# Optimization experiments

Measured on AMD Instinct MI355X. Metric: run time of the kernel, lower is better.

Reference implementation:

```python
import jax, jax.numpy as jnp
import numpy as np

B, A, C, G = 32, 5, 20, 19
TPER = 8  # targets per image -> T = B*TPER = 256
ANCHORS = np.array([[1.3221, 1.73145], [3.19275, 4.00944], [5.05587, 8.09892],
                    [9.47112, 4.84053], [11.2364, 10.0071]], dtype=np.float32)
OBJECT_SCALE, NOOBJECT_SCALE, CLASS_SCALE, COORD_SCALE = 5.0, 1.0, 1.0, 1.0
THRESH = 0.6


def _wh_iou_np(anc, wh):
    inter = np.minimum(anc[:, 0:1], wh[None, :, 0]) * np.minimum(anc[:, 1:2], wh[None, :, 1])
    union = anc[:, 0:1] * anc[:, 1:2] + wh[None, :, 0] * wh[None, :, 1] - inter
    return inter / (union + 1e-16)


def setup_inputs() -> dict:
    rng = np.random.default_rng(0)
    rows = []
    for b in range(B):
        cells = rng.choice(G * G, TPER, replace=False)  # distinct grid cells per image
        for c in cells:
            gy, gx = divmod(int(c), G)
            u, v = rng.uniform(0.05, 0.95, 2)
            w, h = rng.uniform(1.0, 8.0, 2) / G  # 1..8 grid units, in 0..1 image coords
            rows.append([b, rng.integers(C), (gx + u) / G, (gy + v) / G, w, h])
    t = np.array(rows, dtype=np.float32)
    # sort targets into (sample, anchor, gy, gx) mask order so mask-order gathers
    # line up with target-row order (as the original torch code implicitly assumes)
    wh_g = t[:, 4:6] * G
    ai = np.argmax(_wh_iou_np(ANCHORS, wh_g), axis=0)
    gx = (t[:, 2] * G).astype(np.int64)
    gy = (t[:, 3] * G).astype(np.int64)
    flat = ((t[:, 0].astype(np.int64) * A + ai) * G + gy) * G + gx
    t = t[np.argsort(flat)]
    x = jax.random.normal(jax.random.key(0), (B, A * (C + 5), G, G), dtype=jnp.float32) * 0.5
    return {"x": x, "targets": jnp.asarray(t), "seen": 0}


def _bbox_iou(b1, b2):
    # center-format boxes, last dim = (x, y, w, h); broadcasts over leading dims
    b1x1 = b1[..., 0] - b1[..., 2] / 2; b1x2 = b1[..., 0] + b1[..., 2] / 2
    b1y1 = b1[..., 1] - b1[..., 3] / 2; b1y2 = b1[..., 1] + b1[..., 3] / 2
    b2x1 = b2[..., 0] - b2[..., 2] / 2; b2x2 = b2[..., 0] + b2[..., 2] / 2
    b2y1 = b2[..., 1] - b2[..., 3] / 2; b2y2 = b2[..., 1] + b2[..., 3] / 2
    iw = jnp.clip(jnp.minimum(b1x2, b2x2) - jnp.maximum(b1x1, b2x1), 0.0)
    ih = jnp.clip(jnp.minimum(b1y2, b2y2) - jnp.maximum(b1y1, b2y1), 0.0)
    inter = iw * ih
    union = b1[..., 2] * b1[..., 3] + b2[..., 2] * b2[..., 3] - inter
    return inter / (union + 1e-16)


def _forward(x, targets, seen):
    anchors = jnp.asarray(ANCHORS)
    xp = x.reshape(B, A, C + 5, G, G).transpose(0, 1, 3, 4, 2)  # (B,A,G,G,C+5)
    tx, ty, tw, th = xp[..., 0], xp[..., 1], xp[..., 2], xp[..., 3]
    pred_conf = jax.nn.sigmoid(xp[..., 4])
    pred_cls = jax.nn.sigmoid(xp[..., 5:])
    tgs = targets[:, 2:6] * G  # (T,4) in grid units
    # anchor assignment via wh-iou (argmax over anchors)
    inter = jnp.minimum(anchors[:, 0:1], tgs[None, :, 2]) * jnp.minimum(anchors[:, 1:2], tgs[None, :, 3])
    wh_iou = inter / (anchors[:, 0:1] * anchors[:, 1:2] + tgs[None, :, 2] * tgs[None, :, 3] - inter)
    ai = jnp.argmax(wh_iou, axis=0)
    gx = tgs[:, 0].astype(jnp.int32); gy = tgs[:, 1].astype(jnp.int32)
    si = targets[:, 0].astype(jnp.int32); ci = targets[:, 1].astype(jnp.int32)
    # decode full grid
    gridx = jnp.arange(G, dtype=x.dtype)[None, None, None, :]
    gridy = jnp.arange(G, dtype=x.dtype)[None, None, :, None]
    sx, sy = jax.nn.sigmoid(tx), jax.nn.sigmoid(ty)
    pw = jnp.exp(tw) * anchors[:, 0][None, :, None, None]
    ph = jnp.exp(th) * anchors[:, 1][None, :, None, None]
    pred_boxes = jnp.stack([sx + gridx, sy + gridy, pw, ph], axis=-1)  # (B,A,G,G,4)
    T = targets.shape[0]
    target_mask = jnp.zeros((B, A, G, G), bool).at[si, ai, gy, gx].set(True)
    # losses at the T target locations (targets pre-sorted into mask order)
    iou_t = _bbox_iou(pred_boxes[si, ai, gy, gx], tgs)  # (T,)
    loss_cls = jnp.mean((pred_cls[si, ai, gy, gx] - jax.nn.one_hot(ci, C, dtype=x.dtype)) ** 2) * CLASS_SCALE
    tconf = iou_t  # rescore == 1: target_conf = 1 * iou
    loss_obj = jnp.mean((pred_conf[si, ai, gy, gx] - tconf) ** 2) * OBJECT_SCALE
    tcoords = jnp.stack([tgs[:, 0] - gx, tgs[:, 1] - gy,
                         jnp.log(tgs[:, 2] / anchors[ai, 0]),
                         jnp.log(tgs[:, 3] / anchors[ai, 1])], axis=-1)  # (T,4)
    pcoords_t = jnp.stack([sx[si, ai, gy, gx], sy[si, ai, gy, gx],
                           tw[si, ai, gy, gx], th[si, ai, gy, gx]], axis=-1)
    scale = jnp.sqrt(2.0 - tgs[:, 2] * tgs[:, 3] / (G * G))[:, None]
    loss_coords = jnp.mean(((pcoords_t - tcoords) * scale) ** 2) * COORD_SCALE
    # noobject mask: any-target IoU > thresh suppresses the noobj penalty (chunked over targets)
    CHUNK = 32
    tchunks = tgs.reshape(T // CHUNK, CHUNK, 4)
    def body(mx, tc):
        iou = _bbox_iou(pred_boxes[None], tc[:, None, None, None, None, :])  # (CHUNK,B,A,G,G)
        return jnp.maximum(mx, iou.max(0)), None
    max_iou, _ = jax.lax.scan(body, jnp.zeros((B, A, G, G), x.dtype), tchunks)
    noobj = (~target_mask) & (max_iou <= THRESH)
    ncnt = jnp.sum(noobj)
    loss_noobj = jnp.sum(jnp.where(noobj, pred_conf ** 2, 0.0)) / ncnt * NOOBJECT_SCALE
    total = loss_cls + loss_obj + loss_coords + loss_noobj
    if seen < 12800:
        prior = jnp.array([0.5, 0.5, 0.0, 0.0], x.dtype)
        pcoords = jnp.stack([sx, sy, tw, th], axis=-1)  # (B,A,G,G,4)
        nm = ~target_mask
        loss_prior = jnp.sum(jnp.where(nm[..., None], (pcoords - prior) ** 2, 0.0)) / (jnp.sum(nm) * 4) * 0.01
        total = total + loss_prior
    return total


def reference(x, targets, seen):
    return _forward(x, targets, seen)
```

## Files before the change

kernel.cpp:

```cpp
#include <hip/hip_runtime.h>
#include <math.h>

#define NB 32
#define NA 5
#define NC 20
#define NG 19
#define NT 256
#define GG  (NG*NG)
#define CELLS (NB*NA*NG*NG)
#define CPB 64
#define NBLK ((CELLS + CPB - 1)/CPB)
#define NWAVE 4
#define NTHR 256

#define OBJECT_SCALE   5.0f
#define NOOBJ_SCALE    1.0f
#define CLASS_SCALE    1.0f
#define COORD_SCALE    1.0f

__constant__ float c_aw[5] = {1.3221f, 3.19275f, 5.05587f, 9.47112f, 11.2364f};
__constant__ float c_ah[5] = {1.73145f, 4.00944f, 8.09892f, 4.84053f, 10.0071f};

__device__ __forceinline__ float sigm(float v) { return 1.f / (1.f + expf(-v)); }

#define SUMS_OFF 0
#define PART_OFF 16

__global__ __launch_bounds__(NTHR)
void k_main(const float* __restrict__ x, const float* __restrict__ tg,
            float* __restrict__ ws_f, float* __restrict__ partials) {
    __shared__ float4 s_corn[NT];
    __shared__ float  s_s06[NT];
    __shared__ int    s_mask[CPB];
    __shared__ float  s_pm[NWAVE][CPB];
    __shared__ float  s_wred[12];

    const int t = threadIdx.x;
    const int wave = t >> 6, lane = t & 63;
    const int cellBase = blockIdx.x * CPB;
    const int idx = cellBase + lane;
    const bool valid = idx < CELLS;

    float txv = 0.f, tyv = 0.f, twv = 0.f, thv = 0.f, cfv = 0.f;
    int ca = 0, cgx = 0, cgy = 0;
    if (valid) {
        int gx = idx % NG;
        int r  = idx / NG;
        int gy = r % NG;  r /= NG;
        int a  = r % NA;
        int b  = r / NA;
        ca = a; cgx = gx; cgy = gy;
        int base = ((b*NA + a)*(NC+5))*GG + gy*NG + gx;
        txv = x[base + 0*GG];
        tyv = x[base + 1*GG];
        twv = x[base + 2*GG];
        thv = x[base + 3*GG];
        cfv = x[base + 4*GG];
    }
    if (t < CPB) s_mask[t] = 0;

    const float2* tg2 = (const float2*)tg;
    float2 p0 = tg2[t*3+0], p1 = tg2[t*3+1], p2 = tg2[t*3+2];
    const float gxf = p1.x * NG, gyf = p1.y * NG;
    const float gw  = p2.x * NG, gh  = p2.y * NG;
    const int si = (int)p0.x, ci = (int)p0.y;
    int ai = 0;
    {
        float best = -1.f;
        #pragma unroll
        for (int a = 0; a < NA; ++a) {
            float inter = fminf(c_aw[a], gw) * fminf(c_ah[a], gh);
            float uni   = c_aw[a]*c_ah[a] + gw*gh - inter;
            float iou   = inter / uni;
            if (iou > best) { best = iou; ai = a; }
        }
    }
    const int gxi = (int)gxf, gyi = (int)gyf;
    const int fid = ((si*NA + ai)*NG + gyi)*NG + gxi;
    {
        float hw = gw*0.5f, hh = gh*0.5f;
        s_corn[t] = make_float4(gxf - hw, gyf - hh, gxf + hw, gyf + hh);
        s_s06[t]  = 0.6f * (gw * gh);
    }
    __syncthreads();

    {
        int rel = fid - cellBase;
        if (rel >= 0 && rel < CPB) s_mask[rel] = 1;
    }
    float bx1 = 1e30f, by1 = 1e30f, bx2 = 1e30f, by2 = 1e30f, cthr = 0.f;
    float sx = 0.f, sy = 0.f;
    if (valid) {
        sx = sigm(txv); sy = sigm(tyv);
        float pw = expf(twv) * c_aw[ca], ph = expf(thv) * c_ah[ca];
        float cx = sx + (float)cgx, cy = sy + (float)cgy;
        bx1 = cx - pw*0.5f; bx2 = cx + pw*0.5f;
        by1 = cy - ph*0.5f; by2 = cy + ph*0.5f;
        cthr = 0.6f * (pw * ph) + 6e-17f;
    }
    __syncthreads();

    float m0 = -1e30f, m1 = -1e30f;
    #pragma unroll 8
    for (int i = 0; i < 32; ++i) {
        int j0 = (i << 3) + wave;
        int j1 = j0 + 4;
        float4 ta = s_corn[j0];
        float sa = s_s06[j0];
        float4 tb = s_corn[j1];
        float sb = s_s06[j1];
        float iwa = fmaxf(fminf(bx2, ta.z) - fmaxf(bx1, ta.x), 0.f);
        float iha = fmaxf(fminf(by2, ta.w) - fmaxf(by1, ta.y), 0.f);
        float iwb = fmaxf(fminf(bx2, tb.z) - fmaxf(bx1, tb.x), 0.f);
        float ihb = fmaxf(fminf(by2, tb.w) - fmaxf(by1, tb.y), 0.f);
        m0 = fmaxf(m0, fmaf(1.6f, iwa * iha, -sa));
        m1 = fmaxf(m1, fmaf(1.6f, iwb * ihb, -sb));
    }
    s_pm[wave][lane] = fmaxf(m0, m1);
    __syncthreads();

    if (wave == 0) {
        float mm = fmaxf(fmaxf(s_pm[0][lane], s_pm[1][lane]),
                         fmaxf(s_pm[2][lane], s_pm[3][lane]));
        float v_no = 0.f, v_nc = 0.f, v_pr = 0.f, v_nm = 0.f;
        if (valid && !s_mask[lane]) {
            v_nm = 1.f;
            float e0 = sx - 0.5f, e1 = sy - 0.5f;
            v_pr = e0*e0 + e1*e1 + twv*twv + thv*thv;
            if (!(mm > cthr)) {
                float pc = sigm(cfv);
                v_no = pc * pc;
                v_nc = 1.f;
            }
        }
        #pragma unroll
        for (int off = 32; off > 0; off >>= 1) {
            v_no += __shfl_down(v_no, off);
            v_nc += __shfl_down(v_nc, off);
            v_pr += __shfl_down(v_pr, off);
            v_nm += __shfl_down(v_nm, off);
        }
        if (lane == 0) {
            partials[blockIdx.x*4 + 0] = v_no;
            partials[blockIdx.x*4 + 1] = v_nc;
            partials[blockIdx.x*4 + 2] = v_pr;
            partials[blockIdx.x*4 + 3] = v_nm;
        }
    }

    if (blockIdx.x == 0) {
        int base = ((si*NA + ai)*(NC+5))*GG + gyi*NG + gxi;
        float txt = x[base + 0*GG];
        float tyt = x[base + 1*GG];
        float twt = x[base + 2*GG];
        float tht = x[base + 3*GG];
        float cft = x[base + 4*GG];
        float tsx = sigm(txt), tsy = sigm(tyt);
        float aw = c_aw[ai], ah = c_ah[ai];
        float pw = expf(twt) * aw, ph = expf(tht) * ah;

        float pcx = tsx + (float)gxi, pcy = tsy + (float)gyi;
        float hw = gw*0.5f, hh = gh*0.5f;
        float iw = fmaxf(0.f, fminf(pcx + pw*0.5f, gxf + hw) - fmaxf(pcx - pw*0.5f, gxf - hw));
        float ih = fmaxf(0.f, fminf(pcy + ph*0.5f, gyf + hh) - fmaxf(pcy - ph*0.5f, gyf - hh));
        float inter = iw * ih;
        float uni = pw*ph + gw*gh - inter;
        float iou = inter / (uni + 1e-16f);

        float pconf = sigm(cft);
        float dobj = pconf - iou;
        float s_obj = dobj * dobj;

        float s_cls = 0.f;
        for (int cc = 0; cc < NC; ++cc) {
            float pc = sigm(x[base + (5 + cc)*GG]);
            float d = pc - ((cc == ci) ? 1.f : 0.f);
            s_cls += d * d;
        }

        float scl = sqrtf(2.f - gw*gh / (float)(NG*NG));
        float d0 = (tsx - (gxf - (float)gxi)) * scl;
        float d1 = (tsy - (gyf - (float)gyi)) * scl;
        float d2 = (twt - logf(gw / aw)) * scl;
        float d3 = (tht - logf(gh / ah)) * scl;
        float s_crd = d0*d0 + d1*d1 + d2*d2 + d3*d3;

        #pragma unroll
        for (int off = 32; off > 0; off >>= 1) {
            s_cls += __shfl_down(s_cls, off);
            s_obj += __shfl_down(s_obj, off);
            s_crd += __shfl_down(s_crd, off);
        }
        if (lane == 0) {
            s_wred[wave*3 + 0] = s_cls;
            s_wred[wave*3 + 1] = s_obj;
            s_wred[wave*3 + 2] = s_crd;
        }
        __syncthreads();
        if (t == 0) {
            ws_f[SUMS_OFF + 0] = s_wred[0] + s_wred[3] + s_wred[6] + s_wred[9];
            ws_f[SUMS_OFF + 1] = s_wred[1] + s_wred[4] + s_wred[7] + s_wred[10];
            ws_f[SUMS_OFF + 2] = s_wred[2] + s_wred[5] + s_wred[8] + s_wred[11];
        }
    }
}

__global__ __launch_bounds__(256)
void k_final(const float* __restrict__ ws_f, const float* __restrict__ partials,
             const int* __restrict__ seen, float* __restrict__ out) {
    int t = threadIdx.x;
    float a0 = 0.f, a1 = 0.f, a2 = 0.f, a3 = 0.f;
    for (int j = t; j < NBLK; j += 256) {
        a0 += partials[j*4 + 0];
        a1 += partials[j*4 + 1];
        a2 += partials[j*4 + 2];
        a3 += partials[j*4 + 3];
    }
    __shared__ float r0[256], r1[256], r2[256], r3[256];
    r0[t] = a0; r1[t] = a1; r2[t] = a2; r3[t] = a3;
    __syncthreads();
    for (int s = 128; s > 0; s >>= 1) {
        if (t < s) { r0[t]+=r0[t+s]; r1[t]+=r1[t+s]; r2[t]+=r2[t+s]; r3[t]+=r3[t+s]; }
        __syncthreads();
    }
    if (t == 0) {
        float loss_cls = ws_f[SUMS_OFF + 0] / (float)(NT * NC) * CLASS_SCALE;
        float loss_obj = ws_f[SUMS_OFF + 1] / (float)NT * OBJECT_SCALE;
        float loss_crd = ws_f[SUMS_OFF + 2] / (float)(NT * 4) * COORD_SCALE;
        float loss_no  = r0[0] / r1[0] * NOOBJ_SCALE;
        float total = loss_cls + loss_obj + loss_crd + loss_no;
        if (seen[0] < 12800) {
            total += r2[0] / (r3[0] * 4.f) * 0.01f;
        }
        out[0] = total;
    }
}

extern "C" void kernel_launch(void* const* d_in, const int* in_sizes, int n_in,
                              void* d_out, int out_size, void* d_ws, size_t ws_size,
                              hipStream_t stream) {
    const float* x    = (const float*)d_in[0];
    const float* tg   = (const float*)d_in[1];
    const int*   seen = (const int*)d_in[2];
    float* out  = (float*)d_out;
    float* ws_f = (float*)d_ws;
    float* partials = ws_f + PART_OFF;

    k_main<<<NBLK, NTHR, 0, stream>>>(x, tg, ws_f, partials);
    k_final<<<1, 256, 0, stream>>>(ws_f, partials, seen, out);
}
```

Measured before the change: 18.45 us.

## Double waves per block for IoU scan and use shuffle reduction in final kernel

Raises the main kernel from 4 to 8 waves per 64-cell block, so each wave scans half as many targets in the max-IoU loop. Only the first 256 threads load targets and compute target losses. The anchor argmax now compares by cross-multiplication instead of dividing. The final kernel reads partials as float4 and reduces with wave shuffles instead of a shared-memory tree. The trade-off is larger blocks with more idle threads in the target phases, which may lower occupancy.

```diff
diff --git a/kernel.cpp b/kernel.cpp
--- a/kernel.cpp
+++ b/kernel.cpp
@@ -10,8 +10,8 @@
 #define CELLS (NB*NA*NG*NG)
 #define CPB 64
 #define NBLK ((CELLS + CPB - 1)/CPB)
-#define NWAVE 4
-#define NTHR 256
+#define NWAVE 8
+#define NTHR (NWAVE*64)
 
 #define OBJECT_SCALE   5.0f
 #define NOOBJ_SCALE    1.0f
@@ -59,32 +59,32 @@
     }
     if (t < CPB) s_mask[t] = 0;
 
-    const float2* tg2 = (const float2*)tg;
-    float2 p0 = tg2[t*3+0], p1 = tg2[t*3+1], p2 = tg2[t*3+2];
-    const float gxf = p1.x * NG, gyf = p1.y * NG;
-    const float gw  = p2.x * NG, gh  = p2.y * NG;
-    const int si = (int)p0.x, ci = (int)p0.y;
-    int ai = 0;
-    {
-        float best = -1.f;
+    float gxf = 0.f, gyf = 0.f, gw = 0.f, gh = 0.f;
+    int si = 0, ci = 0, ai = 0, gxi = 0, gyi = 0, fid = -1;
+    if (t < NT) {
+        const float2* tg2 = (const float2*)tg;
+        float2 p0 = tg2[t*3+0], p1 = tg2[t*3+1], p2 = tg2[t*3+2];
+        gxf = p1.x * NG; gyf = p1.y * NG;
+        gw  = p2.x * NG; gh  = p2.y * NG;
+        si = (int)p0.x; ci = (int)p0.y;
+        float tarea = gw * gh;
+        float b_inter = fminf(c_aw[0], gw) * fminf(c_ah[0], gh);
+        float b_uni   = c_aw[0]*c_ah[0] + tarea - b_inter;
         #pragma unroll
-        for (int a = 0; a < NA; ++a) {
+        for (int a = 1; a < NA; ++a) {
             float inter = fminf(c_aw[a], gw) * fminf(c_ah[a], gh);
-            float uni   = c_aw[a]*c_ah[a] + gw*gh - inter;
-            float iou   = inter / uni;
-            if (iou > best) { best = iou; ai = a; }
-        }
-    }
-    const int gxi = (int)gxf, gyi = (int)gyf;
-    const int fid = ((si*NA + ai)*NG + gyi)*NG + gxi;
-    {
+            float uni   = c_aw[a]*c_ah[a] + tarea - inter;
+            if (inter * b_uni > b_inter * uni) { b_inter = inter; b_uni = uni; ai = a; }
+        }
+        gxi = (int)gxf; gyi = (int)gyf;
+        fid = ((si*NA + ai)*NG + gyi)*NG + gxi;
         float hw = gw*0.5f, hh = gh*0.5f;
         s_corn[t] = make_float4(gxf - hw, gyf - hh, gxf + hw, gyf + hh);
-        s_s06[t]  = 0.6f * (gw * gh);
-    }
-    __syncthreads();
-
-    {
+        s_s06[t]  = 0.6f * tarea;
+    }
+    __syncthreads();
+
+    if (t < NT) {
         int rel = fid - cellBase;
         if (rel >= 0 && rel < CPB) s_mask[rel] = 1;
     }
@@ -101,10 +101,10 @@
     __syncthreads();
 
     float m0 = -1e30f, m1 = -1e30f;
-    #pragma unroll 8
-    for (int i = 0; i < 32; ++i) {
-        int j0 = (i << 3) + wave;
-        int j1 = j0 + 4;
+    #pragma unroll
+    for (int i = 0; i < 16; ++i) {
+        int j0 = (i << 4) + wave;
+        int j1 = j0 + 8;
         float4 ta = s_corn[j0];
         float sa = s_s06[j0];
         float4 tb = s_corn[j1];
@@ -120,8 +120,9 @@
     __syncthreads();
 
     if (wave == 0) {
-        float mm = fmaxf(fmaxf(s_pm[0][lane], s_pm[1][lane]),
-                         fmaxf(s_pm[2][lane], s_pm[3][lane]));
+        float mm = s_pm[0][lane];
+        #pragma unroll
+        for (int w = 1; w < NWAVE; ++w) mm = fmaxf(mm, s_pm[w][lane]);
         float v_no = 0.f, v_nc = 0.f, v_pr = 0.f, v_nm = 0.f;
         if (valid && !s_mask[lane]) {
             v_nm = 1.f;
@@ -149,52 +150,54 @@
     }
 
     if (blockIdx.x == 0) {
-        int base = ((si*NA + ai)*(NC+5))*GG + gyi*NG + gxi;
-        float txt = x[base + 0*GG];
-        float tyt = x[base + 1*GG];
-        float twt = x[base + 2*GG];
-        float tht = x[base + 3*GG];
-        float cft = x[base + 4*GG];
-        float tsx = sigm(txt), tsy = sigm(tyt);
-        float aw = c_aw[ai], ah = c_ah[ai];
-        float pw = expf(twt) * aw, ph = expf(tht) * ah;
-
-        float pcx = tsx + (float)gxi, pcy = tsy + (float)gyi;
-        float hw = gw*0.5f, hh = gh*0.5f;
-        float iw = fmaxf(0.f, fminf(pcx + pw*0.5f, gxf + hw) - fmaxf(pcx - pw*0.5f, gxf - hw));
-        float ih = fmaxf(0.f, fminf(pcy + ph*0.5f, gyf + hh) - fmaxf(pcy - ph*0.5f, gyf - hh));
-        float inter = iw * ih;
-        float uni = pw*ph + gw*gh - inter;
-        float iou = inter / (uni + 1e-16f);
-
-        float pconf = sigm(cft);
-        float dobj = pconf - iou;
-        float s_obj = dobj * dobj;
-
-        float s_cls = 0.f;
-        for (int cc = 0; cc < NC; ++cc) {
-            float pc = sigm(x[base + (5 + cc)*GG]);
-            float d = pc - ((cc == ci) ? 1.f : 0.f);
-            s_cls += d * d;
-        }
-
-        float scl = sqrtf(2.f - gw*gh / (float)(NG*NG));
-        float d0 = (tsx - (gxf - (float)gxi)) * scl;
-        float d1 = (tsy - (gyf - (float)gyi)) * scl;
-        float d2 = (twt - logf(gw / aw)) * scl;
-        float d3 = (tht - logf(gh / ah)) * scl;
-        float s_crd = d0*d0 + d1*d1 + d2*d2 + d3*d3;
-
-        #pragma unroll
-        for (int off = 32; off > 0; off >>= 1) {
-            s_cls += __shfl_down(s_cls, off);
-            s_obj += __shfl_down(s_obj, off);
-            s_crd += __shfl_down(s_crd, off);
-        }
-        if (lane == 0) {
-            s_wred[wave*3 + 0] = s_cls;
-            s_wred[wave*3 + 1] = s_obj;
-            s_wred[wave*3 + 2] = s_crd;
+        float s_cls = 0.f, s_obj = 0.f, s_crd = 0.f;
+        if (t < NT) {
+            int base = ((si*NA + ai)*(NC+5))*GG + gyi*NG + gxi;
+            float txt = x[base + 0*GG];
+            float tyt = x[base + 1*GG];
+            float twt = x[base + 2*GG];
+            float tht = x[base + 3*GG];
+            float cft = x[base + 4*GG];
+            float tsx = sigm(txt), tsy = sigm(tyt);
+            float aw = c_aw[ai], ah = c_ah[ai];
+            float pw = expf(twt) * aw, ph = expf(tht) * ah;
+
+            float pcx = tsx + (float)gxi, pcy = tsy + (float)gyi;
+            float hw = gw*0.5f, hh = gh*0.5f;
+            float iw = fmaxf(0.f, fminf(pcx + pw*0.5f, gxf + hw) - fmaxf(pcx - pw*0.5f, gxf - hw));
+            float ih = fmaxf(0.f, fminf(pcy + ph*0.5f, gyf + hh) - fmaxf(pcy - ph*0.5f, gyf - hh));
+            float inter = iw * ih;
+            float uni = pw*ph + gw*gh - inter;
+            float iou = inter / (uni + 1e-16f);
+
+            float pconf = sigm(cft);
+            float dobj = pconf - iou;
+            s_obj = dobj * dobj;
+
+            for (int cc = 0; cc < NC; ++cc) {
+                float pc = sigm(x[base + (5 + cc)*GG]);
+                float d = pc - ((cc == ci) ? 1.f : 0.f);
+                s_cls += d * d;
+            }
+
+            float scl = sqrtf(2.f - gw*gh / (float)(NG*NG));
+            float d0 = (tsx - (gxf - (float)gxi)) * scl;
+            float d1 = (tsy - (gyf - (float)gyi)) * scl;
+            float d2 = (twt - logf(gw / aw)) * scl;
+            float d3 = (tht - logf(gh / ah)) * scl;
+            s_crd = d0*d0 + d1*d1 + d2*d2 + d3*d3;
+
+            #pragma unroll
+            for (int off = 32; off > 0; off >>= 1) {
+                s_cls += __shfl_down(s_cls, off);
+                s_obj += __shfl_down(s_obj, off);
+                s_crd += __shfl_down(s_crd, off);
+            }
+            if (lane == 0) {
+                s_wred[wave*3 + 0] = s_cls;
+                s_wred[wave*3 + 1] = s_obj;
+                s_wred[wave*3 + 2] = s_crd;
+            }
         }
         __syncthreads();
         if (t == 0) {
@@ -208,29 +211,38 @@
 __global__ __launch_bounds__(256)
 void k_final(const float* __restrict__ ws_f, const float* __restrict__ partials,
              const int* __restrict__ seen, float* __restrict__ out) {
+    const float4* p4 = (const float4*)partials;
     int t = threadIdx.x;
     float a0 = 0.f, a1 = 0.f, a2 = 0.f, a3 = 0.f;
     for (int j = t; j < NBLK; j += 256) {
-        a0 += partials[j*4 + 0];
-        a1 += partials[j*4 + 1];
-        a2 += partials[j*4 + 2];
-        a3 += partials[j*4 + 3];
-    }
-    __shared__ float r0[256], r1[256], r2[256], r3[256];
-    r0[t] = a0; r1[t] = a1; r2[t] = a2; r3[t] = a3;
-    __syncthreads();
-    for (int s = 128; s > 0; s >>= 1) {
-        if (t < s) { r0[t]+=r0[t+s]; r1[t]+=r1[t+s]; r2[t]+=r2[t+s]; r3[t]+=r3[t+s]; }
-        __syncthreads();
-    }
+        float4 v = p4[j];
+        a0 += v.x; a1 += v.y; a2 += v.z; a3 += v.w;
+    }
+    #pragma unroll
+    for (int off = 32; off > 0; off >>= 1) {
+        a0 += __shfl_down(a0, off);
+        a1 += __shfl_down(a1, off);
+        a2 += __shfl_down(a2, off);
+        a3 += __shfl_down(a3, off);
+    }
+    __shared__ float s_w[4][4];
+    int wave = t >> 6, lane = t & 63;
+    if (lane == 0) {
+        s_w[wave][0] = a0; s_w[wave][1] = a1; s_w[wave][2] = a2; s_w[wave][3] = a3;
+    }
+    __syncthreads();
     if (t == 0) {
+        float r0 = s_w[0][0] + s_w[1][0] + s_w[2][0] + s_w[3][0];
+        float r1 = s_w[0][1] + s_w[1][1] + s_w[2][1] + s_w[3][1];
+        float r2 = s_w[0][2] + s_w[1][2] + s_w[2][2] + s_w[3][2];
+        float r3 = s_w[0][3] + s_w[1][3] + s_w[2][3] + s_w[3][3];
         float loss_cls = ws_f[SUMS_OFF + 0] / (float)(NT * NC) * CLASS_SCALE;
         float loss_obj = ws_f[SUMS_OFF + 1] / (float)NT * OBJECT_SCALE;
         float loss_crd = ws_f[SUMS_OFF + 2] / (float)(NT * 4) * COORD_SCALE;
-        float loss_no  = r0[0] / r1[0] * NOOBJ_SCALE;
+        float loss_no  = r0 / r1 * NOOBJ_SCALE;
         float total = loss_cls + loss_obj + loss_crd + loss_no;
         if (seen[0] < 12800) {
-            total += r2[0] / (r3[0] * 4.f) * 0.01f;
+            total += r2 / (r3 * 4.f) * 0.01f;
         }
         out[0] = total;
     }
```

After: 17.71 us. 4.0% less time.
